# Kernel tuning notes

Hardware: AMD Instinct MI355X
Metric: run time of the kernel (lower is better)

Reference implementation:

```python
import jax, jax.numpy as jnp
import numpy as np

# ---- static dims (must match setup_inputs) ----
B = 32          # graphs per batch
NX_PER = 1024   # encoder nodes per graph
NY_PER = 512    # SLT nodes per graph
NX, NY = B * NX_PER, B * NY_PER
E = 65536       # SLT edges
F = 256         # f_size (encoder feature dim)
EMB = 256       # emb_size
H = 512         # h_size
VOCAB = 512
NT = 4          # len(SltEdgeTypes)
NREL = 7        # len(SrtEdgeTypes)


def setup_inputs() -> dict:
    key = jax.random.key(0)
    ks = jax.random.split(key, 20)
    p = lambda i, shape: (jax.random.normal(ks[i], shape, jnp.float32) * 0.02)
    return {
        'x': jax.random.normal(ks[0], (NX, F), jnp.float32),
        'tgt_y': jax.random.randint(ks[1], (NY,), 0, VOCAB),
        'tgt_edge_index': jax.random.randint(ks[2], (2, E), 0, NY),
        'tgt_edge_type': jax.random.randint(ks[3], (E,), 0, NT),
        'x_batch': jnp.repeat(jnp.arange(B), NX_PER),   # uniform, sorted
        'y_batch': jnp.repeat(jnp.arange(B), NY_PER),
        'embed_table': p(4, (VOCAB, EMB)),
        'Wz': p(5, (EMB, VOCAB)), 'bz': jnp.zeros((VOCAB,), jnp.float32),
        'Wg': p(6, (2 * EMB, NREL)), 'bg': jnp.zeros((NREL,), jnp.float32),
        'We1': p(7, (NT, EMB, H)), 'Wq1': p(8, (EMB, F)), 'Wc1': p(9, (F, H)), 'b1': jnp.zeros((H,), jnp.float32),
        'We2': p(10, (NT, H, H)), 'Wq2': p(11, (H, F)), 'Wc2': p(12, (F, H)), 'b2': jnp.zeros((H,), jnp.float32),
        'We3': p(13, (NT, H, EMB)), 'Wq3': p(14, (H, F)), 'Wc3': p(15, (F, EMB)), 'b3': jnp.zeros((EMB,), jnp.float32),
    }


def _gcn_dec_layer(x_b, y, ei, et, We, Wq, Wc, b):
    """GCN attention decoder layer: per-edge-type linear message passing over
    the SLT edges + batch-masked dot-product attention over encoder nodes x.
    x_b: [B, nx, F]; y: [NY, in]. Returns ([NY, out], alpha [B, ny, nx])."""
    # edge-type-specific projection, then gather per edge (cheap: 4 GEMMs)
    proj = jnp.einsum('ni,tio->tno', y, We)           # [NT, NY, out]
    msg = proj[et, ei[0]]                              # [E, out] irregular gather
    agg = jax.ops.segment_sum(msg, ei[1], num_segments=y.shape[0])  # [NY, out]
    # cross attention y -> x (within each graph; uniform sorted batches)
    q = (y @ Wq).reshape(B, NY_PER, F)                 # [B, ny, F]
    scores = jnp.einsum('bqf,bkf->bqk', q, x_b) / jnp.sqrt(jnp.float32(F))
    alpha = jax.nn.softmax(scores, axis=-1)            # [B, ny, nx]
    ctx = jnp.einsum('bqk,bkf->bqf', alpha, x_b).reshape(NY, F)
    out = jax.nn.relu(agg + ctx @ Wc + b)
    return out, alpha


def reference(x, tgt_y, tgt_edge_index, tgt_edge_type, x_batch, y_batch,
              embed_table, Wz, bz, Wg, bg,
              We1, Wq1, Wc1, b1, We2, Wq2, Wc2, b2, We3, Wq3, Wc3, b3):
    x_b = x.reshape(B, NX_PER, F)
    y0 = embed_table[tgt_y]                            # embedding lookup [NY, EMB]
    embeds_out = y0 @ Wz + bz                          # lin_z_out on raw embeds
    y1, a1 = _gcn_dec_layer(x_b, y0, tgt_edge_index, tgt_edge_type, We1, Wq1, Wc1, b1)
    y2, a2 = _gcn_dec_layer(x_b, y1, tgt_edge_index, tgt_edge_type, We2, Wq2, Wc2, b2)
    y3, a3 = _gcn_dec_layer(x_b, y2, tgt_edge_index, tgt_edge_type, We3, Wq3, Wc3, b3)
    y_score = y3 @ Wz + bz                             # [NY, VOCAB]
    # y[y_edge_index].permute(1,0,2).flatten(1) == concat(src_feats, dst_feats)
    ef = jnp.concatenate([y3[tgt_edge_index[0]], y3[tgt_edge_index[1]]], axis=1)  # [E, 2*EMB]
    y_edge_rel_score = ef @ Wg + bg                    # [E, NREL]
    return (y3, tgt_edge_index, tgt_edge_type, y_score, y_edge_rel_score,
            embeds_out, a1, a2, a3)
```

## Files before the change

kernel.cpp:

```cpp
#include <hip/hip_runtime.h>

#define B_G   32
#define NXP   1024
#define NYP   512
#define NX_T  32768
#define NY_T  16384
#define E_T   65536
#define F_SZ  256
#define EMB_S 256
#define H_SZ  512
#define VOC   512

static const long O_Y3  = 0;
static const long O_EI  = 4194304;
static const long O_ET  = 4325376;
static const long O_YS  = 4390912;
static const long O_REL = 12779520;
static const long O_EMB = 13238272;
static const long O_A1  = 21626880;
static const long O_A2  = 38404096;
static const long O_A3  = 55181312;

using bf16x8 = __attribute__((ext_vector_type(8))) __bf16;
using f32x4  = __attribute__((ext_vector_type(4))) float;

__device__ __forceinline__ ushort f2bf(float f) {
  union { float f; unsigned u; } v; v.f = f;
  return (ushort)((v.u + 0x7FFFu + ((v.u >> 16) & 1u)) >> 16);
}
__device__ __forceinline__ float bf2f(ushort s) {
  union { unsigned u; float f; } v; v.u = ((unsigned)s) << 16;
  return v.f;
}

__device__ __forceinline__ void g2l16(const ushort* g, ushort* l) {
  __builtin_amdgcn_global_load_lds(
      (const __attribute__((address_space(1))) void*)g,
      (__attribute__((address_space(3))) void*)l, 16, 0, 0);
}

struct GemmP {
  const ushort* A; const ushort* Bt;
  float* outF; ushort* outB; float* outF2; ushort* outB2;
  const float* addC; const float* bias; const float* rowScale;
  long sA, sBt, sOutF, sOutB, sAddC, sRS;
  int lda, ldb, ldoF, ldoB, ldoF2, ldoB2, ldC;
  int M, N, K, nSplit;
  float scale; int relu; int expf_;
};

template<int BN>
__global__ __launch_bounds__(256) void gemm_k(GemmP p) {
  constexpr int WGM = (BN == 128) ? 2 : 4;
  constexpr int WGN = (BN == 128) ? 2 : 1;
  constexpr int MT  = 128 / (16 * WGM);
  constexpr int NT  = BN / (16 * WGN);
  constexpr int NCB = (BN * 8) / 256;
  constexpr int ASZ = 128 * 64;
  constexpr int BSZ = BN * 64;
  __shared__ __align__(16) ushort As[2 * ASZ];
  __shared__ __align__(16) ushort Bs[2 * BSZ];
  const int tid  = threadIdx.x;
  const int wave = tid >> 6, lane = tid & 63;

  const int GM = gridDim.x, GN = gridDim.y;
  const int L = blockIdx.x + GM * (blockIdx.y + GN * blockIdx.z);
  const int npan = GM * gridDim.z;
  const int q8 = npan >> 3;
  const int xcd = L & 7;
  const int i = L >> 3;
  const int bnn = i % GN;
  const int panel = xcd * q8 + i / GN;
  const int bmi = panel % GM;
  const int z = panel / GM;
  const int bm = bmi * 128, bn = bnn * BN;

  const ushort* A  = p.A  + (long)z * p.sA;
  const ushort* Bt = p.Bt + (long)z * p.sBt;

  const int wm = (wave / WGN) * (MT * 16);
  const int wn = (wave % WGN) * (NT * 16);
  const int lrow = lane & 15, hg = lane >> 4;
  const int e3 = lrow & 7;

  const ushort* pa[4]; int ca[4];
  const ushort* pb[NCB]; int cb[NCB];
#pragma unroll
  for (int q = 0; q < 4; ++q) {
    const int c = tid + 256 * q, row = c >> 3, sg = (c & 7) ^ (row & 7);
    pa[q] = A + (long)(bm + row) * p.lda + sg * 8;
    ca[q] = c * 8;
  }
#pragma unroll
  for (int q = 0; q < NCB; ++q) {
    const int c = tid + 256 * q, row = c >> 3, sg = (c & 7) ^ (row & 7);
    pb[q] = Bt + (long)(bn + row) * p.ldb + sg * 8;
    cb[q] = c * 8;
  }

  auto stage = [&](int t, int buf) {
    const int ke = t * 64;
#pragma unroll
    for (int q = 0; q < 4; ++q) g2l16(pa[q] + ke, &As[buf * ASZ + ca[q]]);
#pragma unroll
    for (int q = 0; q < NCB; ++q) g2l16(pb[q] + ke, &Bs[buf * BSZ + cb[q]]);
  };

  f32x4 acc[MT][NT];
#pragma unroll
  for (int m = 0; m < MT; ++m)
#pragma unroll
    for (int n = 0; n < NT; ++n) acc[m][n] = f32x4{0.f, 0.f, 0.f, 0.f};

  stage(0, 0);
  __syncthreads();
  const int nt = p.K >> 6;
  int cur = 0;
  for (int t = 0; t < nt; ++t) {
    if (t + 1 < nt) stage(t + 1, cur ^ 1);
    bf16x8 af[MT][2], bf[NT][2];
#pragma unroll
    for (int m = 0; m < MT; ++m) {
      const int rb = cur * ASZ + (wm + m * 16 + lrow) * 64;
#pragma unroll
      for (int kf = 0; kf < 2; ++kf)
        af[m][kf] = *(const bf16x8*)&As[rb + ((((kf << 2) | hg) ^ e3) << 3)];
    }
#pragma unroll
    for (int n = 0; n < NT; ++n) {
      const int rb = cur * BSZ + (wn + n * 16 + lrow) * 64;
#pragma unroll
      for (int kf = 0; kf < 2; ++kf)
        bf[n][kf] = *(const bf16x8*)&Bs[rb + ((((kf << 2) | hg) ^ e3) << 3)];
    }
#pragma unroll
    for (int m = 0; m < MT; ++m)
#pragma unroll
      for (int n = 0; n < NT; ++n) {
        acc[m][n] = __builtin_amdgcn_mfma_f32_16x16x32_bf16(bf[n][0], af[m][0], acc[m][n], 0, 0, 0);
        acc[m][n] = __builtin_amdgcn_mfma_f32_16x16x32_bf16(bf[n][1], af[m][1], acc[m][n], 0, 0, 0);
      }
    __syncthreads();
    cur ^= 1;
  }

  const int rr0 = hg * 4;
#pragma unroll
  for (int m = 0; m < MT; ++m) {
    const long mr = bm + wm + m * 16 + lrow;
    const float rs = p.rowScale ? p.rowScale[(long)z * p.sRS + mr] : 1.0f;
#pragma unroll
    for (int n = 0; n < NT; ++n) {
      const int nc = bn + wn + n * 16 + rr0;
      float vv[4];
#pragma unroll
      for (int j = 0; j < 4; ++j) vv[j] = acc[m][n][j] * p.scale;
      if (nc < p.nSplit) {
        if (p.expf_) {
#pragma unroll
          for (int j = 0; j < 4; ++j) vv[j] = __expf(vv[j]);
        }
#pragma unroll
        for (int j = 0; j < 4; ++j) vv[j] *= rs;
        if (p.addC) {
          float4 c4 = *(const float4*)&p.addC[(long)z * p.sAddC + mr * p.ldC + nc];
          vv[0] += c4.x; vv[1] += c4.y; vv[2] += c4.z; vv[3] += c4.w;
        }
        if (p.bias) {
          float4 b4 = *(const float4*)&p.bias[nc];
          vv[0] += b4.x; vv[1] += b4.y; vv[2] += b4.z; vv[3] += b4.w;
        }
        if (p.relu) {
#pragma unroll
          for (int j = 0; j < 4; ++j) vv[j] = fmaxf(vv[j], 0.f);
        }
        if (p.outF) {
          float4 o4 = make_float4(vv[0], vv[1], vv[2], vv[3]);
          *(float4*)&p.outF[(long)z * p.sOutF + mr * p.ldoF + nc] = o4;
        }
        if (p.outB) {
          ushort4 ob;
          ob.x = f2bf(vv[0]); ob.y = f2bf(vv[1]); ob.z = f2bf(vv[2]); ob.w = f2bf(vv[3]);
          *(ushort4*)&p.outB[(long)z * p.sOutB + mr * p.ldoB + nc] = ob;
        }
      } else {
        const int nc2 = nc - p.nSplit;
        if (p.outF2 && nc2 < p.ldoF2) {
          float4 o4 = make_float4(vv[0], vv[1], vv[2], vv[3]);
          *(float4*)&p.outF2[mr * (long)p.ldoF2 + nc2] = o4;
        }
        if (p.outB2 && nc2 < p.ldoB2) {
          ushort4 ob;
          ob.x = f2bf(vv[0]); ob.y = f2bf(vv[1]); ob.z = f2bf(vv[2]); ob.w = f2bf(vv[3]);
          *(ushort4*)&p.outB2[mr * (long)p.ldoB2 + nc2] = ob;
        }
      }
    }
  }
}

struct TD { const float* src; ushort* dst; int K; int N; int ldD; };
struct TDs { TD d[22]; };
__global__ __launch_bounds__(256) void t32_k(TDs t) {
  TD d = t.d[blockIdx.z];
  const int k0 = blockIdx.x * 32, n0 = blockIdx.y * 32;
  if (k0 >= d.K || n0 >= d.N) return;
  __shared__ float tl[32][33];
  const int tx = threadIdx.x & 31, ty = threadIdx.x >> 5;
#pragma unroll
  for (int r = ty; r < 32; r += 8)
    if (k0 + r < d.K && n0 + tx < d.N)
      tl[r][tx] = d.src[(long)(k0 + r) * d.N + n0 + tx];
  __syncthreads();
#pragma unroll
  for (int r = ty; r < 32; r += 8)
    if (n0 + r < d.N && k0 + tx < d.K)
      d.dst[(long)(n0 + r) * d.ldD + k0 + tx] = f2bf(tl[tx][r]);
}

__global__ __launch_bounds__(256) void prepx_k(const float* x, ushort* xb, ushort* xT) {
  __shared__ float t[32][33];
  int b = blockIdx.z;
  int j0 = blockIdx.x * 32, f0 = blockIdx.y * 32;
  int tx = threadIdx.x & 31, ty = threadIdx.x >> 5;
#pragma unroll
  for (int r = ty; r < 32; r += 8) {
    float v = x[((long)b * NXP + j0 + r) * F_SZ + f0 + tx];
    t[r][tx] = v;
    xb[((long)b * NXP + j0 + r) * F_SZ + f0 + tx] = f2bf(v);
  }
  __syncthreads();
#pragma unroll
  for (int r = ty; r < 32; r += 8)
    xT[((long)b * F_SZ + f0 + r) * NXP + j0 + tx] = f2bf(t[tx][r]);
}

__global__ void gather_k(const float* emb, const int* tgt_y, ushort* y0b) {
  long i = (long)blockIdx.x * 256 + threadIdx.x;
  int n = (int)(i >> 6), c = (int)(i & 63) * 4;
  int row = tgt_y[n];
  float4 v = *(const float4*)&emb[(long)row * EMB_S + c];
  ushort4 o; o.x = f2bf(v.x); o.y = f2bf(v.y); o.z = f2bf(v.z); o.w = f2bf(v.w);
  *(ushort4*)&y0b[(long)n * EMB_S + c] = o;
}

__global__ __launch_bounds__(256) void rowsum_k(const ushort* E, float* aF, float* inv) {
  __shared__ float red[4];
  const long row = blockIdx.x;
  const int tid = threadIdx.x, lane = tid & 63, wave = tid >> 6;
  const ushort* e = E + row * 1024;
  ushort4 u = *(const ushort4*)&e[tid * 4];
  float v0 = bf2f(u.x), v1 = bf2f(u.y), v2 = bf2f(u.z), v3 = bf2f(u.w);
  float s = (v0 + v1) + (v2 + v3);
#pragma unroll
  for (int o = 32; o; o >>= 1) s += __shfl_xor(s, o, 64);
  if (lane == 0) red[wave] = s;
  __syncthreads();
  float iv = 1.0f / (red[0] + red[1] + red[2] + red[3]);
  float4 a; a.x = v0 * iv; a.y = v1 * iv; a.z = v2 * iv; a.w = v3 * iv;
  *(float4*)&aF[row * 1024 + tid * 4] = a;
  if (tid == 0) inv[row] = iv;
}

__global__ void deg_k(const int* ei, int* cnt) {
  int e = blockIdx.x * 256 + threadIdx.x;
  atomicAdd(&cnt[ei[E_T + e]], 1);
}

__global__ __launch_bounds__(256) void scan_k(const int* cnt, int* ofs, int* cur) {
  __shared__ int sh[256];
  const int t = threadIdx.x;
  int s = 0;
  for (int i = 0; i < 64; ++i) s += cnt[t * 64 + i];
  sh[t] = s; __syncthreads();
  for (int d = 1; d < 256; d <<= 1) {
    int v = (t >= d) ? sh[t - d] : 0;
    __syncthreads();
    sh[t] += v;
    __syncthreads();
  }
  int run = sh[t] - s;
  for (int i = 0; i < 64; ++i) {
    int v = cnt[t * 64 + i];
    ofs[t * 64 + i] = run; cur[t * 64 + i] = run;
    run += v;
  }
  if (t == 255) ofs[16384] = run;
}

__global__ void fill_k(const int* ei, const int* et, int* cur, ushort* adj) {
  int e = blockIdx.x * 256 + threadIdx.x;
  int d = ei[E_T + e];
  int pos = atomicAdd(&cur[d], 1);
  adj[pos] = (ushort)(ei[e] | (et[e] << 14));
}

__global__ __launch_bounds__(256) void gather_y_k(const ushort* y, const ushort* adj,
                                                  const int* ofs, ushort* Abuf,
                                                  int ni, int ldA) {
  const int tpr = ni >> 3;
  const int r = blockIdx.x * (256 / tpr) + threadIdx.x / tpr;
  const int c = (threadIdx.x % tpr) * 8;
  const int s0 = ofs[r], s1 = ofs[r + 1];
  float A0[8], A1[8], A2[8], A3[8];
#pragma unroll
  for (int j = 0; j < 8; ++j) { A0[j] = 0.f; A1[j] = 0.f; A2[j] = 0.f; A3[j] = 0.f; }
  for (int i = s0; i < s1; ++i) {
    const unsigned ad = adj[i];
    const int src = ad & 0x3FFF, t = ad >> 14;
    int4 u = *(const int4*)&y[(long)src * ni + c];
    const ushort* us = (const ushort*)&u;
    if (t == 0) {
#pragma unroll
      for (int j = 0; j < 8; ++j) A0[j] += bf2f(us[j]);
    } else if (t == 1) {
#pragma unroll
      for (int j = 0; j < 8; ++j) A1[j] += bf2f(us[j]);
    } else if (t == 2) {
#pragma unroll
      for (int j = 0; j < 8; ++j) A2[j] += bf2f(us[j]);
    } else {
#pragma unroll
      for (int j = 0; j < 8; ++j) A3[j] += bf2f(us[j]);
    }
  }
  ushort* d = &Abuf[(long)r * ldA + c];
  int4 o; ushort* os = (ushort*)&o;
#pragma unroll
  for (int j = 0; j < 8; ++j) os[j] = f2bf(A0[j]);
  *(int4*)&d[0] = o;
#pragma unroll
  for (int j = 0; j < 8; ++j) os[j] = f2bf(A1[j]);
  *(int4*)&d[ni] = o;
#pragma unroll
  for (int j = 0; j < 8; ++j) os[j] = f2bf(A2[j]);
  *(int4*)&d[2 * ni] = o;
#pragma unroll
  for (int j = 0; j < 8; ++j) os[j] = f2bf(A3[j]);
  *(int4*)&d[3 * ni] = o;
}

__global__ void erel_k(const float* Gbuf, const int* ei, const float* bg, float* outR) {
  long idx = (long)blockIdx.x * 256 + threadIdx.x;
  int e = (int)(idx / 7), r = (int)(idx - (long)e * 7);
  outR[idx] = Gbuf[(long)ei[e] * 16 + r] + Gbuf[(long)ei[E_T + e] * 16 + 7 + r] + bg[r];
}

__global__ void icopy_k(const int* ei, const int* et, float* oEI, float* oET) {
  int idx = blockIdx.x * 256 + threadIdx.x;
  if (idx < 2 * E_T) oEI[idx] = (float)ei[idx];
  else oET[idx - 2 * E_T] = (float)et[idx - 2 * E_T];
}

static GemmP mkp(const ushort* A, long sA, int lda,
                 const ushort* Bt, long sBt, int ldb,
                 int M, int N, int K,
                 float* outF, long sOF, int ldoF,
                 ushort* outB, long sOB, int ldoB,
                 const float* addC, long sC, int ldC,
                 const float* bias, float scale, int relu,
                 int expf_, const float* rowScale, long sRS) {
  GemmP p{};
  p.A = A; p.Bt = Bt; p.outF = outF; p.outB = outB; p.outF2 = nullptr; p.outB2 = nullptr;
  p.addC = addC; p.bias = bias; p.rowScale = rowScale;
  p.sA = sA; p.sBt = sBt; p.sOutF = sOF; p.sOutB = sOB; p.sAddC = sC; p.sRS = sRS;
  p.lda = lda; p.ldb = ldb; p.ldoF = ldoF; p.ldoB = ldoB; p.ldoF2 = 0; p.ldoB2 = 0; p.ldC = ldC;
  p.M = M; p.N = N; p.K = K; p.nSplit = 1 << 30;
  p.scale = scale; p.relu = relu; p.expf_ = expf_;
  return p;
}

static void gemm128(hipStream_t st, const GemmP& p, int Z) {
  dim3 grid(p.M / 128, p.N / 128, Z);
  hipLaunchKernelGGL(gemm_k<128>, grid, dim3(256), 0, st, p);
}
static void gemm64(hipStream_t st, const GemmP& p, int Z) {
  dim3 grid(p.M / 128, p.N / 64, Z);
  hipLaunchKernelGGL(gemm_k<64>, grid, dim3(256), 0, st, p);
}

extern "C" void kernel_launch(void* const* d_in, const int* in_sizes, int n_in,
                              void* d_out_, int out_size, void* d_ws, size_t ws_size,
                              hipStream_t stream) {
  const float* x     = (const float*)d_in[0];
  const int*   tgt_y = (const int*)d_in[1];
  const int*   ei    = (const int*)d_in[2];
  const int*   et    = (const int*)d_in[3];
  const float* emb   = (const float*)d_in[6];
  const float* Wz    = (const float*)d_in[7];
  const float* bz    = (const float*)d_in[8];
  const float* Wg    = (const float*)d_in[9];
  const float* bg    = (const float*)d_in[10];
  const float* We[3] = {(const float*)d_in[11], (const float*)d_in[15], (const float*)d_in[19]};
  const float* Wq[3] = {(const float*)d_in[12], (const float*)d_in[16], (const float*)d_in[20]};
  const float* Wc[3] = {(const float*)d_in[13], (const float*)d_in[17], (const float*)d_in[21]};
  const float* bb[3] = {(const float*)d_in[14], (const float*)d_in[18], (const float*)d_in[22]};
  float* out = (float*)d_out_;

  ushort* wsu    = (ushort*)d_ws;
  ushort* WzG    = wsu + 0;
  ushort* WzQ1   = wsu + 163840;
  ushort* WB0    = wsu + 360448;
  ushort* WB1    = wsu + 1015808;
  ushort* WB2    = wsu + 2195456;
  ushort* WqT2   = wsu + 2785280;
  ushort* WqT3   = wsu + 2916352;
  ushort* xb     = wsu + 3047424;
  ushort* xTb    = wsu + 11436032;
  ushort* qbuf   = wsu + 19824640;
  ushort* ybuf   = wsu + 24018944;
  ushort* Abuf   = wsu + 32407552;
  ushort* scoreb = wsu + 70156288;
  float*  Gbuf   = (float*)(wsu + 86933504);
  float*  inv    = (float*)(wsu + 91127808);
  float*  bcat   = (float*)(wsu + 91160576);
  int*    cnt    = (int*)(wsu + 91162112);
  int*    ofs    = (int*)(wsu + 91194880);
  int*    cur    = (int*)(wsu + 91227712);
  ushort* adj    = wsu + 91260480;

  ushort* GgT  = WzG + 512 * 256;
  ushort* Wq1T = WzQ1 + 512 * 256;
  ushort* WB[3]  = {WB0, WB1, WB2};
  const int ni_l[3] = {256, 512, 512}, no_l[3] = {512, 512, 256};
  const int ldA_l[3] = {1280, 2304, 2304};

  hipMemcpyAsync(bcat, bz, 512 * sizeof(float), hipMemcpyDeviceToDevice, stream);
  hipMemsetAsync(bcat + 512, 0, 256 * sizeof(float), stream);
  hipMemsetAsync(GgT + 14 * 256, 0, (128 - 14) * 256 * sizeof(ushort), stream);
  hipMemsetAsync(cnt, 0, 16384 * sizeof(int), stream);

  TDs td; int di = 0;
  td.d[di++] = {Wz, WzG, 256, 512, 256};
  td.d[di++] = {Wz, WzQ1, 256, 512, 256};
  td.d[di++] = {Wg, GgT, 256, 7, 256};
  td.d[di++] = {Wg + 256 * 7, GgT + 7 * 256, 256, 7, 256};
  td.d[di++] = {Wq[0], Wq1T, 256, 256, 256};
  for (int l = 0; l < 3; ++l) {
    const int ni = ni_l[l], no = no_l[l], ldA = ldA_l[l];
    for (int t = 0; t < 4; ++t)
      td.d[di++] = {We[l] + (long)t * ni * no, WB[l] + (long)t * ni, ni, no, ldA};
    td.d[di++] = {Wc[l], WB[l] + (long)4 * ni, 256, no, ldA};
    if (l > 0) td.d[di++] = {Wq[l], (l == 1) ? WqT2 : WqT3, ni, 256, ni};
  }
  hipLaunchKernelGGL(t32_k, dim3(16, 16, 22), dim3(256), 0, stream, td);

  hipLaunchKernelGGL(prepx_k, dim3(32, 8, 32), dim3(256), 0, stream, x, xb, xTb);
  hipLaunchKernelGGL(gather_k, dim3(4096), dim3(256), 0, stream, emb, tgt_y, ybuf);

  hipLaunchKernelGGL(deg_k, dim3(256), dim3(256), 0, stream, ei, cnt);
  hipLaunchKernelGGL(scan_k, dim3(1), dim3(256), 0, stream, cnt, ofs, cur);
  hipLaunchKernelGGL(fill_k, dim3(256), dim3(256), 0, stream, ei, et, cur, adj);

  {
    GemmP p = mkp(ybuf, 0, 256, WzQ1, 0, 256, NY_T, 768, 256,
                  out + O_EMB, 0, 512, nullptr, 0, 0,
                  nullptr, 0, 0, bcat, 1.0f, 0, 0, nullptr, 0);
    p.nSplit = 512; p.outB2 = qbuf; p.ldoB2 = 256;
    gemm128(stream, p, 1);
  }

  float* alphaO[3] = {out + O_A1, out + O_A2, out + O_A3};
  ushort* WqTn[3] = {nullptr, WqT2, WqT3};

  for (int l = 0; l < 3; ++l) {
    const int ni = ni_l[l], no = no_l[l], ldA = ldA_l[l];
    if (l > 0) {
      GemmP p = mkp(ybuf, 0, ni, WqTn[l], 0, ni, NY_T, 256, ni,
                    nullptr, 0, 0, qbuf, 0, 256,
                    nullptr, 0, 0, nullptr, 1.0f, 0, 0, nullptr, 0);
      gemm64(stream, p, 1);
    }
    hipLaunchKernelGGL(gather_y_k, dim3(NY_T / (256 / (ni >> 3))), dim3(256), 0, stream,
                       ybuf, adj, ofs, Abuf, ni, ldA);
    {
      GemmP p = mkp(qbuf, (long)512 * 256, 256, xb, (long)1024 * 256, 256,
                    512, 1024, 256, nullptr, 0, 0, scoreb, (long)512 * 1024, 1024,
                    nullptr, 0, 0, nullptr, 0.0625f, 0, 1, nullptr, 0);
      gemm128(stream, p, 32);
    }
    hipLaunchKernelGGL(rowsum_k, dim3(16384), dim3(256), 0, stream, scoreb, alphaO[l], inv);
    {
      GemmP p = mkp(scoreb, (long)512 * 1024, 1024, xTb, (long)256 * 1024, 1024,
                    512, 256, 1024, nullptr, 0, 0, Abuf + 4 * ni, (long)512 * ldA, ldA,
                    nullptr, 0, 0, nullptr, 1.0f, 0, 0, inv, 512);
      gemm64(stream, p, 32);
    }
    {
      GemmP p = mkp(Abuf, 0, ldA, WB[l], 0, ldA, NY_T, no, ldA,
                    (l == 2) ? out + O_Y3 : nullptr, 0, no, ybuf, 0, no,
                    nullptr, 0, 0, bb[l], 1.0f, 1, 0, nullptr, 0);
      if (no == 256) gemm64(stream, p, 1); else gemm128(stream, p, 1);
    }
  }

  {
    GemmP p = mkp(ybuf, 0, 256, WzG, 0, 256, NY_T, 640, 256,
                  out + O_YS, 0, 512, nullptr, 0, 0,
                  nullptr, 0, 0, bcat, 1.0f, 0, 0, nullptr, 0);
    p.nSplit = 512; p.outF2 = Gbuf; p.ldoF2 = 16;
    gemm128(stream, p, 1);
  }
  hipLaunchKernelGGL(erel_k, dim3(1792), dim3(256), 0, stream, Gbuf, ei, bg, out + O_REL);
  hipLaunchKernelGGL(icopy_k, dim3(768), dim3(256), 0, stream, ei, et, out + O_EI, out + O_ET);
}
```

Before: 562.5 us.

## Deepen GEMM prefetch to two tiles with explicit waitcnt and fuse tail kernels

The GEMM main loop now issues global-to-LDS loads two k-tiles ahead. It uses explicit vmcnt waits and raw barriers in place of the single-stage prefetch followed by a full __syncthreads, so memory latency can overlap more MFMA work. The next stage is issued only after the LDS fragment reads are complete, which frees the buffer for reuse. Separately, the edge relation-score kernel and the index copy kernel are merged into one launch to save launch overhead. The hand-written vmcnt counts depend on how many loads each stage issues, so if they do not match the compiler's output the result can be wrong or the kernel can stall.

Measured after the change: 537.8 us. 4.4% less time.

```diff
diff --git a/kernel.cpp b/kernel.cpp
--- a/kernel.cpp
+++ b/kernel.cpp
@@ -113,11 +113,18 @@
     for (int n = 0; n < NT; ++n) acc[m][n] = f32x4{0.f, 0.f, 0.f, 0.f};
 
   stage(0, 0);
-  __syncthreads();
+  stage(1, 1);
   const int nt = p.K >> 6;
   int cur = 0;
   for (int t = 0; t < nt; ++t) {
-    if (t + 1 < nt) stage(t + 1, cur ^ 1);
+    if (t + 1 < nt) {
+      if constexpr (BN == 128) asm volatile("s_waitcnt vmcnt(8)" ::: "memory");
+      else                     asm volatile("s_waitcnt vmcnt(6)" ::: "memory");
+    } else {
+      asm volatile("s_waitcnt vmcnt(0)" ::: "memory");
+    }
+    __builtin_amdgcn_s_barrier();
+    __builtin_amdgcn_sched_barrier(0);
     bf16x8 af[MT][2], bf[NT][2];
 #pragma unroll
     for (int m = 0; m < MT; ++m) {
@@ -133,6 +140,11 @@
       for (int kf = 0; kf < 2; ++kf)
         bf[n][kf] = *(const bf16x8*)&Bs[rb + ((((kf << 2) | hg) ^ e3) << 3)];
     }
+    asm volatile("s_waitcnt lgkmcnt(0)" ::: "memory");
+    __builtin_amdgcn_sched_barrier(0);
+    __builtin_amdgcn_s_barrier();
+    __builtin_amdgcn_sched_barrier(0);
+    if (t + 2 < nt) stage(t + 2, cur);
 #pragma unroll
     for (int m = 0; m < MT; ++m)
 #pragma unroll
@@ -140,7 +152,6 @@
         acc[m][n] = __builtin_amdgcn_mfma_f32_16x16x32_bf16(bf[n][0], af[m][0], acc[m][n], 0, 0, 0);
         acc[m][n] = __builtin_amdgcn_mfma_f32_16x16x32_bf16(bf[n][1], af[m][1], acc[m][n], 0, 0, 0);
       }
-    __syncthreads();
     cur ^= 1;
   }
 
@@ -340,16 +351,18 @@
   *(int4*)&d[3 * ni] = o;
 }
 
-__global__ void erel_k(const float* Gbuf, const int* ei, const float* bg, float* outR) {
+__global__ void erelic_k(const float* Gbuf, const int* ei, const int* et,
+                         const float* bg, float* outR, float* oEI, float* oET) {
+  const long nrel = (long)E_T * 7;
   long idx = (long)blockIdx.x * 256 + threadIdx.x;
-  int e = (int)(idx / 7), r = (int)(idx - (long)e * 7);
-  outR[idx] = Gbuf[(long)ei[e] * 16 + r] + Gbuf[(long)ei[E_T + e] * 16 + 7 + r] + bg[r];
-}
-
-__global__ void icopy_k(const int* ei, const int* et, float* oEI, float* oET) {
-  int idx = blockIdx.x * 256 + threadIdx.x;
-  if (idx < 2 * E_T) oEI[idx] = (float)ei[idx];
-  else oET[idx - 2 * E_T] = (float)et[idx - 2 * E_T];
+  if (idx < nrel) {
+    int e = (int)(idx / 7), r = (int)(idx - (long)e * 7);
+    outR[idx] = Gbuf[(long)ei[e] * 16 + r] + Gbuf[(long)ei[E_T + e] * 16 + 7 + r] + bg[r];
+  } else {
+    long j = idx - nrel;
+    if (j < 2 * E_T) oEI[j] = (float)ei[j];
+    else if (j < 3 * E_T) oET[j - 2 * E_T] = (float)et[j - 2 * E_T];
+  }
 }
 
 static GemmP mkp(const ushort* A, long sA, int lda,
@@ -501,6 +514,6 @@
     p.nSplit = 512; p.outF2 = Gbuf; p.ldoF2 = 16;
     gemm128(stream, p, 1);
   }
-  hipLaunchKernelGGL(erel_k, dim3(1792), dim3(256), 0, stream, Gbuf, ei, bg, out + O_REL);
-  hipLaunchKernelGGL(icopy_k, dim3(768), dim3(256), 0, stream, ei, et, out + O_EI, out + O_ET);
-}
+  hipLaunchKernelGGL(erelic_k, dim3(2560), dim3(256), 0, stream,
+                     Gbuf, ei, et, bg, out + O_REL, out + O_EI, out + O_ET);
+}
```
